# Kernel optimization log

Measured on AMD Instinct MI355X. Metric: run time of the kernel, lower is better.

Reference implementation:

```python
import jax, jax.numpy as jnp
import numpy as np

EPS = 1e-7
LN_EPS = 1e-5

# Lorentz model, points represented by spatial coords x in R^dim; time coord t = sqrt(K + ||x||^2), K = 1/c.

def log_map_zero(x, c):
    K = 1.0 / c
    sqrtK = jnp.sqrt(K)
    xnorm = jnp.linalg.norm(x, axis=-1, keepdims=True)
    t = jnp.sqrt(K + xnorm * xnorm)
    theta = jnp.arccosh(jnp.maximum(t / sqrtK, 1.0 + EPS))
    return sqrtK * theta * x / jnp.maximum(xnorm, EPS)


def exp_map_zero(v, c):
    K = 1.0 / c
    sqrtK = jnp.sqrt(K)
    vnorm = jnp.linalg.norm(v, axis=-1, keepdims=True)
    return sqrtK * jnp.sinh(vnorm / sqrtK) * v / jnp.maximum(vnorm, EPS)


def layer_norm(x, gamma, beta):
    mu = jnp.mean(x, axis=-1, keepdims=True)
    var = jnp.mean((x - mu) ** 2, axis=-1, keepdims=True)
    return (x - mu) * jax.lax.rsqrt(var + LN_EPS) * gamma + beta


def setup_inputs() -> dict:
    key = jax.random.key(0)
    N, D, E, L = 50000, 128, 800000, 2
    ks = jax.random.split(key, 8)
    x_hyp = jax.random.normal(ks[0], (N, D), dtype=jnp.float32)
    edge_index = jax.random.randint(ks[1], (2, E), 0, N, dtype=jnp.int64)
    W = jax.random.normal(ks[2], (L, D, D), dtype=jnp.float32) / np.sqrt(D)
    b = jnp.zeros((L, D), dtype=jnp.float32)
    gamma = jnp.ones((L, D), dtype=jnp.float32)
    beta = jnp.zeros((L, D), dtype=jnp.float32)
    curv = jnp.ones((L,), dtype=jnp.float32)
    return {"x_hyp": x_hyp, "edge_index": edge_index, "W": W, "b": b,
            "gamma": gamma, "beta": beta, "curv": curv}


def reference(x_hyp, edge_index, W, b, gamma, beta, curv):
    N = x_hyp.shape[0]
    L = W.shape[0]
    src, dst = edge_index[0], edge_index[1]
    # in-degree counts for mean aggregation (clamped to avoid div by 0)
    counts = jax.ops.segment_sum(jnp.ones_like(dst, dtype=x_hyp.dtype), dst, num_segments=N)
    counts = jnp.maximum(counts, 1.0)[:, None]
    x = x_hyp
    for l in range(L):
        # curvature treated as constant (torch uses .item())
        c = jax.lax.stop_gradient(jnp.clip(curv[l], 0.1, 10.0))
        x_tan = log_map_zero(x, c)                      # [N, D]
        x_lin = x_tan @ W[l].T + b[l]                   # [N, D]
        msgs = x_lin[src]                               # [E, D] gather
        agg = jax.ops.segment_sum(msgs, dst, num_segments=N) / counts  # scatter-mean
        x_tan_out = layer_norm(x_tan + agg, gamma[l], beta[l])  # dropout in eval mode
        x = exp_map_zero(x_tan_out, c)
    return x
```

## Files before the change

### kernel.cpp

```cpp
#include <hip/hip_runtime.h>
#include <hip/hip_bf16.h>

typedef __attribute__((ext_vector_type(4))) float f32x4;
typedef __attribute__((ext_vector_type(2))) float f32x2;
typedef __attribute__((ext_vector_type(8))) short bf16x8;

constexpr int D = 128;
constexpr int SB = 256;
constexpr int K4CAP = 8192;
#define FEPS 1e-7f
#define FLN_EPS 1e-5f

__device__ __forceinline__ float groupReduceSum16(float x) {
#pragma unroll
  for (int off = 1; off < 16; off <<= 1) x += __shfl_xor(x, off, 64);
  return x;
}

__device__ __forceinline__ unsigned short f2bf(float x) {
  unsigned int u = __float_as_uint(x);
  u += 0x7fffu + ((u >> 16) & 1u);
  return (unsigned short)(u >> 16);
}

__device__ __forceinline__ unsigned int pack2(float a, float b) {
  return (unsigned int)f2bf(a) | ((unsigned int)f2bf(b) << 16);
}

__device__ __forceinline__ f32x2 unp(unsigned int x) {
  f32x2 r;
  r.x = __uint_as_float(x << 16);
  r.y = __uint_as_float(x & 0xffff0000u);
  return r;
}

__device__ __forceinline__ void accp(f32x2* A, uint4 u) {
  A[0] += unp(u.x);
  A[1] += unp(u.y);
  A[2] += unp(u.z);
  A[3] += unp(u.w);
}


__global__ __launch_bounds__(1024) void k2_scan(int* __restrict__ bh,
                                                int* __restrict__ bucket_base, int NB, int E) {
  __shared__ int bsum[256];
  int tid = threadIdx.x, lane = tid & 63, wv = tid >> 6;
  for (int bin = wv; bin < NB; bin += 16) {
    int carry = 0;
    int* row = bh + bin * SB;
#pragma unroll
    for (int sgm = 0; sgm < 4; ++sgm) {
      int v = row[sgm * 64 + lane];
      int x = v;
#pragma unroll
      for (int off = 1; off < 64; off <<= 1) {
        int t = __shfl_up(x, off, 64);
        if (lane >= off) x += t;
      }
      row[sgm * 64 + lane] = carry + x - v;
      carry += __shfl(x, 63, 64);
    }
    if (lane == 0) bsum[bin] = carry;
  }
  __syncthreads();
  if (wv == 0) {
    int carry = 0;
    for (int base = 0; base < NB; base += 64) {
      int v = (base + lane < NB) ? bsum[base + lane] : 0;
      int x = v;
#pragma unroll
      for (int off = 1; off < 64; off <<= 1) {
        int t = __shfl_up(x, off, 64);
        if (lane >= off) x += t;
      }
      if (base + lane < NB) {
        int excl = carry + x - v;
        bsum[base + lane] = excl;
        bucket_base[base + lane] = excl;
      }
      carry += __shfl(x, 63, 64);
    }
    if (lane == 0) bucket_base[NB] = E;
  }
  __syncthreads();
  for (int bin = wv; bin < NB; bin += 16) {
    int bb = bsum[bin];
    int* row = bh + bin * SB;
    for (int s = lane; s < SB; s += 64) row[s] += bb;
  }
}

__global__ __launch_bounds__(1024) void k3_scatter(const int* __restrict__ src,
                                                   const int* __restrict__ dst,
                                                   const int* __restrict__ bh,
                                                   unsigned int* __restrict__ ebuf, int E,
                                                   int NB, int chunk) {
  __shared__ int base[256];
  __shared__ int cur[256];
  int tid = threadIdx.x;
  if (tid < 256) {
    base[tid] = (tid < NB) ? bh[tid * SB + blockIdx.x] : 0;
    cur[tid] = 0;
  }
  __syncthreads();
  int e0 = blockIdx.x * chunk;
  int e1 = min(e0 + chunk, E);
  for (int e = e0 + tid; e < e1; e += 1024) {
    int d = dst[e];
    int s = src[e];
    int bin = d >> 8;
    int r = atomicAdd(&cur[bin], 1);
    ebuf[base[bin] + r] = (unsigned int)(s & 0xffff) | ((unsigned int)(d & 255) << 16);
  }
}

__global__ __launch_bounds__(1024) void k4_csr(const unsigned int* __restrict__ ebuf,
                                               const int* __restrict__ bucket_base,
                                               int* __restrict__ rowptr,
                                               unsigned short* __restrict__ col, int N, int NB,
                                               int E) {
  __shared__ unsigned int stash[K4CAP];
  __shared__ int hist[256];
  __shared__ int cur[256];
  int b = blockIdx.x, tid = threadIdx.x;
  int e0 = bucket_base[b], e1 = bucket_base[b + 1];
  int cnt = e1 - e0;
  if (tid < 256) {
    hist[tid] = 0;
    cur[tid] = 0;
  }
  __syncthreads();
  for (int i = tid; i < cnt; i += 1024) {
    unsigned int u = ebuf[e0 + i];
    if (i < K4CAP) stash[i] = u;
    atomicAdd(&hist[u >> 16], 1);
  }
  __syncthreads();
  int lane = tid & 63;
  if (tid < 64) {
    int carry = 0;
#pragma unroll
    for (int sgm = 0; sgm < 4; ++sgm) {
      int v = hist[sgm * 64 + lane];
      int x = v;
#pragma unroll
      for (int off = 1; off < 64; off <<= 1) {
        int t = __shfl_up(x, off, 64);
        if (lane >= off) x += t;
      }
      hist[sgm * 64 + lane] = carry + x - v;
      carry += __shfl(x, 63, 64);
    }
  }
  __syncthreads();
  int node0 = b << 8;
  if (tid < 256 && node0 + tid < N) rowptr[node0 + tid] = e0 + hist[tid];
  if (b == 0 && tid == 0) rowptr[N] = E;
  for (int i = tid; i < cnt; i += 1024) {
    unsigned int u = (i < K4CAP) ? stash[i] : ebuf[e0 + i];
    int slot = u >> 16;
    int r = atomicAdd(&cur[slot], 1);
    col[e0 + hist[slot] + r] = (unsigned short)(u & 0xffff);
  }
}


template <int FIRST>
__device__ __forceinline__ void gemm_body1024(int gbid, unsigned short* Wlds,
                                              const float* __restrict__ xf,
                                              const unsigned short* __restrict__ A,
                                              const float* __restrict__ Wf,
                                              const float* __restrict__ bias,
                                              const float* __restrict__ curv, int l,
                                              unsigned short* __restrict__ xt,
                                              unsigned short* __restrict__ xl, int N) {
  const float* Wp = Wf + (size_t)l * D * D;
  for (int idx = threadIdx.x; idx < 2048; idx += 1024) {
    int lanei = idx & 63, kbt = idx >> 6;
    int kb = kbt & 3, tcol = kbt >> 2;
    int g = lanei >> 4, r = lanei & 15;
    const float* s = Wp + (size_t)(tcol * 16 + r) * D + kb * 32 + g * 8;
    float4 f0 = *reinterpret_cast<const float4*>(s);
    float4 f1 = *reinterpret_cast<const float4*>(s + 4);
    uint4 u;
    u.x = pack2(f0.x, f0.y);
    u.y = pack2(f0.z, f0.w);
    u.z = pack2(f1.x, f1.y);
    u.w = pack2(f1.z, f1.w);
    *reinterpret_cast<uint4*>(&Wlds[idx * 8]) = u;
  }
  __syncthreads();
  int lane = threadIdx.x & 63;
  int trow = gbid * 16 + (threadIdx.x >> 6);
  int n0 = trow * 16;
  if (n0 >= N) return;
  int g = lane >> 4, r = lane & 15;
  int ar = n0 + r;
  if (ar > N - 1) ar = N - 1;

  bf16x8 af[4];
  if (FIRST) {
    float c = fminf(fmaxf(curv[l], 0.1f), 10.0f);
    float K = 1.0f / c, sqrtK = sqrtf(K);
    float4 fa[4][2];
    float ss = 0.f;
#pragma unroll
    for (int kb = 0; kb < 4; ++kb) {
      const float4* xr = reinterpret_cast<const float4*>(xf + (size_t)ar * D + kb * 32 + g * 8);
      fa[kb][0] = xr[0];
      fa[kb][1] = xr[1];
      ss += fa[kb][0].x * fa[kb][0].x + fa[kb][0].y * fa[kb][0].y +
            fa[kb][0].z * fa[kb][0].z + fa[kb][0].w * fa[kb][0].w;
      ss += fa[kb][1].x * fa[kb][1].x + fa[kb][1].y * fa[kb][1].y +
            fa[kb][1].z * fa[kb][1].z + fa[kb][1].w * fa[kb][1].w;
    }
    ss += __shfl_xor(ss, 16, 64);
    ss += __shfl_xor(ss, 32, 64);
    float xnorm = sqrtf(ss);
    float t = sqrtf(K + ss);
    float theta = acoshf(fmaxf(t / sqrtK, 1.0f + FEPS));
    float scale = sqrtK * theta / fmaxf(xnorm, FEPS);
#pragma unroll
    for (int kb = 0; kb < 4; ++kb) {
      union { bf16x8 v; uint4 u; } cv;
      cv.u.x = pack2(fa[kb][0].x * scale, fa[kb][0].y * scale);
      cv.u.y = pack2(fa[kb][0].z * scale, fa[kb][0].w * scale);
      cv.u.z = pack2(fa[kb][1].x * scale, fa[kb][1].y * scale);
      cv.u.w = pack2(fa[kb][1].z * scale, fa[kb][1].w * scale);
      af[kb] = cv.v;
      *reinterpret_cast<uint4*>(xt + (size_t)ar * D + kb * 32 + g * 8) = cv.u;
    }
  } else {
#pragma unroll
    for (int kb = 0; kb < 4; ++kb)
      af[kb] = *reinterpret_cast<const bf16x8*>(A + (size_t)ar * D + kb * 32 + g * 8);
  }

  int colj = lane & 15, rb = (lane >> 4) * 4;
#pragma unroll
  for (int tcol = 0; tcol < 8; ++tcol) {
    f32x4 acc = {0.f, 0.f, 0.f, 0.f};
#pragma unroll
    for (int kb = 0; kb < 4; ++kb) {
      bf16x8 bfm = *reinterpret_cast<const bf16x8*>(&Wlds[((tcol * 4 + kb) * 64 + lane) * 8]);
      acc = __builtin_amdgcn_mfma_f32_16x16x32_bf16(af[kb], bfm, acc, 0, 0, 0);
    }
    float bv = bias[l * D + tcol * 16 + colj];
#pragma unroll
    for (int i = 0; i < 4; ++i) {
      int row = n0 + rb + i;
      if (row < N) xl[(size_t)row * D + tcol * 16 + colj] = f2bf(acc[i] + bv);
    }
  }
}

__global__ __launch_bounds__(1024) void fusedA_kernel(const int* __restrict__ dst,
                                                      int* __restrict__ bh, int E, int NB,
                                                      int chunk, const float* __restrict__ xf,
                                                      const float* __restrict__ Wf,
                                                      const float* __restrict__ bias,
                                                      const float* __restrict__ curv,
                                                      unsigned short* __restrict__ xt,
                                                      unsigned short* __restrict__ xl, int N) {
  __shared__ unsigned short Wlds[128 * 128];
  int bid = blockIdx.x;
  if (bid < SB) {
    int* h = (int*)Wlds;
    int tid = threadIdx.x;
    if (tid < 256) h[tid] = 0;
    __syncthreads();
    int e0 = bid * chunk;
    int e1 = min(e0 + chunk, E);
    for (int e = e0 + tid; e < e1; e += 1024) atomicAdd(&h[dst[e] >> 8], 1);
    __syncthreads();
    if (tid < NB) bh[tid * SB + bid] = h[tid];
  } else {
    gemm_body1024<1>(bid - SB, Wlds, xf, nullptr, Wf, bias, curv, 0, xt, xl, N);
  }
}

__global__ __launch_bounds__(1024) void gemm_kernel(const unsigned short* __restrict__ A,
                                                    const float* __restrict__ Wf,
                                                    const float* __restrict__ bias,
                                                    const float* __restrict__ curv, int l,
                                                    unsigned short* __restrict__ xl, int N) {
  __shared__ unsigned short Wlds[128 * 128];
  gemm_body1024<0>(blockIdx.x, Wlds, nullptr, A, Wf, bias, curv, l, nullptr, xl, N);
}


template <int MODE>
__global__ __launch_bounds__(256) void agg_kernel(const unsigned short* __restrict__ xl,
                                                  unsigned short* __restrict__ xt,
                                                  const int* __restrict__ rowptr,
                                                  const unsigned short* __restrict__ col,
                                                  const float* __restrict__ gamma,
                                                  const float* __restrict__ beta,
                                                  const float* __restrict__ curv, int l,
                                                  float* __restrict__ out, int N) {
  int tid = threadIdx.x;
  int lane = tid & 63;
  int gl = lane & 15, g = lane >> 4;
  int wid = tid >> 6;
  int node = blockIdx.x * 16 + wid * 4 + g;
  bool active = node < N;
  int nd = active ? node : N - 1;

  float c = fminf(fmaxf(curv[l], 0.1f), 10.0f);
  float K = 1.0f / c, sqrtK = sqrtf(K);

  int e0 = rowptr[nd], e1 = rowptr[nd + 1];
  int deg = e1 - e0;
  const unsigned short* cb = col + e0;

  f32x2 A0[4], A1[4], A2[4], A3[4];
#pragma unroll
  for (int j = 0; j < 4; ++j) {
    A0[j] = 0.f;
    A1[j] = 0.f;
    A2[j] = 0.f;
    A3[j] = 0.f;
  }

  const uint4* xlp = reinterpret_cast<const uint4*>(xl);
  for (int base = 0; base < deg; base += 16) {
    int cidx = (base + gl < deg) ? (int)cb[base + gl] : 0;
    int m = deg - base;
    if (m > 16) m = 16;
    int k = 0;
    for (; k + 8 <= m; k += 8) {
      uint4 u[8];
#pragma unroll
      for (int t = 0; t < 8; ++t) {
        int s = __shfl(cidx, g * 16 + k + t, 64);
        u[t] = xlp[(size_t)s * 16 + gl];
      }
      accp(A0, u[0]);
      accp(A1, u[1]);
      accp(A2, u[2]);
      accp(A3, u[3]);
      accp(A0, u[4]);
      accp(A1, u[5]);
      accp(A2, u[6]);
      accp(A3, u[7]);
    }
    for (; k + 2 <= m; k += 2) {
      int s0 = __shfl(cidx, g * 16 + k, 64);
      int s1 = __shfl(cidx, g * 16 + k + 1, 64);
      uint4 u0 = xlp[(size_t)s0 * 16 + gl];
      uint4 u1 = xlp[(size_t)s1 * 16 + gl];
      accp(A0, u0);
      accp(A1, u1);
    }
    if (k < m) {
      int s0 = __shfl(cidx, g * 16 + k, 64);
      uint4 u0 = xlp[(size_t)s0 * 16 + gl];
      accp(A0, u0);
    }
  }
  f32x2 AV[4];
#pragma unroll
  for (int j = 0; j < 4; ++j) AV[j] = (A0[j] + A1[j]) + (A2[j] + A3[j]);

  float inv = 1.f / fmaxf((float)deg, 1.f);
  uint4 ut = reinterpret_cast<const uint4*>(xt)[(size_t)nd * 16 + gl];
  f32x2 utv[4];
  utv[0] = unp(ut.x);
  utv[1] = unp(ut.y);
  utv[2] = unp(ut.z);
  utv[3] = unp(ut.w);
  float v[8];
#pragma unroll
  for (int j = 0; j < 4; ++j) {
    v[2 * j] = utv[j].x + AV[j].x * inv;
    v[2 * j + 1] = utv[j].y + AV[j].y * inv;
  }

  float s1 = 0.f, s2 = 0.f;
#pragma unroll
  for (int j = 0; j < 8; ++j) { s1 += v[j]; s2 += v[j] * v[j]; }
  s1 = groupReduceSum16(s1);
  s2 = groupReduceSum16(s2);
  float mu = s1 * (1.f / 128.f);
  float var = fmaxf(s2 * (1.f / 128.f) - mu * mu, 0.f);
  float rstd = rsqrtf(var + FLN_EPS);

  float4 gm0 = *reinterpret_cast<const float4*>(gamma + l * D + gl * 8);
  float4 gm1 = *reinterpret_cast<const float4*>(gamma + l * D + gl * 8 + 4);
  float4 bt0 = *reinterpret_cast<const float4*>(beta + l * D + gl * 8);
  float4 bt1 = *reinterpret_cast<const float4*>(beta + l * D + gl * 8 + 4);
  float y[8];
  y[0] = (v[0] - mu) * rstd * gm0.x + bt0.x;
  y[1] = (v[1] - mu) * rstd * gm0.y + bt0.y;
  y[2] = (v[2] - mu) * rstd * gm0.z + bt0.z;
  y[3] = (v[3] - mu) * rstd * gm0.w + bt0.w;
  y[4] = (v[4] - mu) * rstd * gm1.x + bt1.x;
  y[5] = (v[5] - mu) * rstd * gm1.y + bt1.y;
  y[6] = (v[6] - mu) * rstd * gm1.z + bt1.z;
  y[7] = (v[7] - mu) * rstd * gm1.w + bt1.w;

  float ss = 0.f;
#pragma unroll
  for (int j = 0; j < 8; ++j) ss += y[j] * y[j];
  ss = groupReduceSum16(ss);
  float vn = sqrtf(ss);
  float sc = sqrtK * sinhf(vn / sqrtK) / fmaxf(vn, FEPS);

  if (MODE == 0) {
    if (active) {
      float4 o0, o1;
      o0.x = y[0] * sc; o0.y = y[1] * sc; o0.z = y[2] * sc; o0.w = y[3] * sc;
      o1.x = y[4] * sc; o1.y = y[5] * sc; o1.z = y[6] * sc; o1.w = y[7] * sc;
      float4* op = reinterpret_cast<float4*>(out + (size_t)node * D + gl * 8);
      op[0] = o0;
      op[1] = o1;
    }
  } else {
    float xn = sqrtK * sinhf(vn / sqrtK);
    float c2 = fminf(fmaxf(curv[l + 1], 0.1f), 10.0f);
    float K2 = 1.0f / c2, sqrtK2 = sqrtf(K2);
    float t2 = sqrtf(K2 + xn * xn);
    float theta = acoshf(fmaxf(t2 / sqrtK2, 1.0f + FEPS));
    float sc2 = sqrtK2 * theta / fmaxf(xn, FEPS);
    float st = sc * sc2;
    if (active) {
      uint4 w;
      w.x = pack2(y[0] * st, y[1] * st);
      w.y = pack2(y[2] * st, y[3] * st);
      w.z = pack2(y[4] * st, y[5] * st);
      w.w = pack2(y[6] * st, y[7] * st);
      reinterpret_cast<uint4*>(xt)[(size_t)node * 16 + gl] = w;
    }
  }
}


extern "C" void kernel_launch(void* const* d_in, const int* in_sizes, int n_in,
                              void* d_out, int out_size, void* d_ws, size_t ws_size,
                              hipStream_t stream) {
  const float* x_hyp = (const float*)d_in[0];
  const int* edge = (const int*)d_in[1];
  const float* W = (const float*)d_in[2];
  const float* b = (const float*)d_in[3];
  const float* gamma = (const float*)d_in[4];
  const float* beta = (const float*)d_in[5];
  const float* curv = (const float*)d_in[6];
  float* out = (float*)d_out;
  int N = in_sizes[0] / D;
  int E = in_sizes[1] / 2;
  int L = in_sizes[6];
  const int* src = edge;
  const int* dst = edge + E;

  char* p = (char*)d_ws;
  auto alloc = [&](size_t bytes) {
    char* r = p;
    p += (bytes + 255) & ~(size_t)255;
    return r;
  };
  int NB = (N + 255) >> 8;
  int chunk = (E + SB - 1) / SB;

  int* bh = (int*)alloc((size_t)256 * SB * 4);
  int* bucket_base = (int*)alloc((size_t)(NB + 1) * 4);
  unsigned int* ebuf = (unsigned int*)alloc((size_t)E * 4);
  int* rowptr = (int*)alloc((size_t)(N + 1) * 4);
  unsigned short* colp = (unsigned short*)alloc((size_t)E * 2);
  unsigned short* xt16 = (unsigned short*)alloc((size_t)N * D * 2);
  unsigned short* xl16 = (unsigned short*)alloc((size_t)N * D * 2);

  int g1024 = ((N + 15) / 16 + 15) / 16;

  fusedA_kernel<<<SB + g1024, 1024, 0, stream>>>(dst, bh, E, NB, chunk, x_hyp, W, b, curv,
                                                 xt16, xl16, N);
  k2_scan<<<1, 1024, 0, stream>>>(bh, bucket_base, NB, E);
  k3_scatter<<<SB, 1024, 0, stream>>>(src, dst, bh, ebuf, E, NB, chunk);
  k4_csr<<<NB, 1024, 0, stream>>>(ebuf, bucket_base, rowptr, colp, N, NB, E);

  for (int l = 0; l < L; ++l) {
    if (l > 0) {
      gemm_kernel<<<g1024, 1024, 0, stream>>>(xt16, W, b, curv, l, xl16, N);
    }
    if (l < L - 1) {
      agg_kernel<1><<<(N + 15) / 16, 256, 0, stream>>>(xl16, xt16, rowptr, colp, gamma, beta,
                                                       curv, l, out, N);
    } else {
      agg_kernel<0><<<(N + 15) / 16, 256, 0, stream>>>(xl16, xt16, rowptr, colp, gamma, beta,
                                                       curv, l, out, N);
    }
  }
}
```

Measured before the change: 151.4 us.

## Fuse next-layer GEMM into aggregation epilogue with ping-pong buffers

Removes the separate layer-1 GEMM kernel. The aggregation kernel now stages its 16-node bf16 tangent tile in LDS and runs the MFMA projection for the next layer in its epilogue. Next-layer weights are pre-converted to bf16 by an extra block in the first fused kernel, and ping-pong buffers keep the read and write xl arrays separate. The accumulator layout is also changed to split even and odd lanes, avoiding per-element unpacking shuffles. The cost is a block barrier, LDS use and weight reads from global/L2 in every aggregation block.

```diff
diff --git a/kernel.cpp b/kernel.cpp
--- a/kernel.cpp
+++ b/kernel.cpp
@@ -34,11 +34,24 @@
   return r;
 }
 
-__device__ __forceinline__ void accp(f32x2* A, uint4 u) {
-  A[0] += unp(u.x);
-  A[1] += unp(u.y);
-  A[2] += unp(u.z);
-  A[3] += unp(u.w);
+struct AccSet {
+  f32x2 e0, o0, e1, o1;
+};
+
+__device__ __forceinline__ void accu(AccSet& s, uint4 u) {
+  f32x2 t;
+  t.x = __uint_as_float(u.x << 16);
+  t.y = __uint_as_float(u.y << 16);
+  s.e0 += t;
+  t.x = __uint_as_float(u.x);
+  t.y = __uint_as_float(u.y);
+  s.o0 += t;
+  t.x = __uint_as_float(u.z << 16);
+  t.y = __uint_as_float(u.w << 16);
+  s.e1 += t;
+  t.x = __uint_as_float(u.z);
+  t.y = __uint_as_float(u.w);
+  s.o1 += t;
 }
 
 
@@ -166,16 +179,14 @@
 }
 
 
-template <int FIRST>
-__device__ __forceinline__ void gemm_body1024(int gbid, unsigned short* Wlds,
-                                              const float* __restrict__ xf,
-                                              const unsigned short* __restrict__ A,
-                                              const float* __restrict__ Wf,
-                                              const float* __restrict__ bias,
-                                              const float* __restrict__ curv, int l,
-                                              unsigned short* __restrict__ xt,
-                                              unsigned short* __restrict__ xl, int N) {
-  const float* Wp = Wf + (size_t)l * D * D;
+__device__ __forceinline__ void gemm0_body(int gbid, unsigned short* Wlds,
+                                           const float* __restrict__ xf,
+                                           const float* __restrict__ Wf,
+                                           const float* __restrict__ bias,
+                                           const float* __restrict__ curv,
+                                           unsigned short* __restrict__ xt,
+                                           unsigned short* __restrict__ xl, int N) {
+  const float* Wp = Wf;
   for (int idx = threadIdx.x; idx < 2048; idx += 1024) {
     int lanei = idx & 63, kbt = idx >> 6;
     int kb = kbt & 3, tcol = kbt >> 2;
@@ -200,41 +211,35 @@
   if (ar > N - 1) ar = N - 1;
 
   bf16x8 af[4];
-  if (FIRST) {
-    float c = fminf(fmaxf(curv[l], 0.1f), 10.0f);
-    float K = 1.0f / c, sqrtK = sqrtf(K);
-    float4 fa[4][2];
-    float ss = 0.f;
-#pragma unroll
-    for (int kb = 0; kb < 4; ++kb) {
-      const float4* xr = reinterpret_cast<const float4*>(xf + (size_t)ar * D + kb * 32 + g * 8);
-      fa[kb][0] = xr[0];
-      fa[kb][1] = xr[1];
-      ss += fa[kb][0].x * fa[kb][0].x + fa[kb][0].y * fa[kb][0].y +
-            fa[kb][0].z * fa[kb][0].z + fa[kb][0].w * fa[kb][0].w;
-      ss += fa[kb][1].x * fa[kb][1].x + fa[kb][1].y * fa[kb][1].y +
-            fa[kb][1].z * fa[kb][1].z + fa[kb][1].w * fa[kb][1].w;
-    }
-    ss += __shfl_xor(ss, 16, 64);
-    ss += __shfl_xor(ss, 32, 64);
-    float xnorm = sqrtf(ss);
-    float t = sqrtf(K + ss);
-    float theta = acoshf(fmaxf(t / sqrtK, 1.0f + FEPS));
-    float scale = sqrtK * theta / fmaxf(xnorm, FEPS);
-#pragma unroll
-    for (int kb = 0; kb < 4; ++kb) {
-      union { bf16x8 v; uint4 u; } cv;
-      cv.u.x = pack2(fa[kb][0].x * scale, fa[kb][0].y * scale);
-      cv.u.y = pack2(fa[kb][0].z * scale, fa[kb][0].w * scale);
-      cv.u.z = pack2(fa[kb][1].x * scale, fa[kb][1].y * scale);
-      cv.u.w = pack2(fa[kb][1].z * scale, fa[kb][1].w * scale);
-      af[kb] = cv.v;
-      *reinterpret_cast<uint4*>(xt + (size_t)ar * D + kb * 32 + g * 8) = cv.u;
-    }
-  } else {
-#pragma unroll
-    for (int kb = 0; kb < 4; ++kb)
-      af[kb] = *reinterpret_cast<const bf16x8*>(A + (size_t)ar * D + kb * 32 + g * 8);
+  float c = fminf(fmaxf(curv[0], 0.1f), 10.0f);
+  float K = 1.0f / c, sqrtK = sqrtf(K);
+  float4 fa[4][2];
+  float ss = 0.f;
+#pragma unroll
+  for (int kb = 0; kb < 4; ++kb) {
+    const float4* xr = reinterpret_cast<const float4*>(xf + (size_t)ar * D + kb * 32 + g * 8);
+    fa[kb][0] = xr[0];
+    fa[kb][1] = xr[1];
+    ss += fa[kb][0].x * fa[kb][0].x + fa[kb][0].y * fa[kb][0].y + fa[kb][0].z * fa[kb][0].z +
+          fa[kb][0].w * fa[kb][0].w;
+    ss += fa[kb][1].x * fa[kb][1].x + fa[kb][1].y * fa[kb][1].y + fa[kb][1].z * fa[kb][1].z +
+          fa[kb][1].w * fa[kb][1].w;
+  }
+  ss += __shfl_xor(ss, 16, 64);
+  ss += __shfl_xor(ss, 32, 64);
+  float xnorm = sqrtf(ss);
+  float t = sqrtf(K + ss);
+  float theta = acoshf(fmaxf(t / sqrtK, 1.0f + FEPS));
+  float scale = sqrtK * theta / fmaxf(xnorm, FEPS);
+#pragma unroll
+  for (int kb = 0; kb < 4; ++kb) {
+    union { bf16x8 v; uint4 u; } cv;
+    cv.u.x = pack2(fa[kb][0].x * scale, fa[kb][0].y * scale);
+    cv.u.y = pack2(fa[kb][0].z * scale, fa[kb][0].w * scale);
+    cv.u.z = pack2(fa[kb][1].x * scale, fa[kb][1].y * scale);
+    cv.u.w = pack2(fa[kb][1].z * scale, fa[kb][1].w * scale);
+    af[kb] = cv.v;
+    *reinterpret_cast<uint4*>(xt + (size_t)ar * D + kb * 32 + g * 8) = cv.u;
   }
 
   int colj = lane & 15, rb = (lane >> 4) * 4;
@@ -246,7 +251,7 @@
       bf16x8 bfm = *reinterpret_cast<const bf16x8*>(&Wlds[((tcol * 4 + kb) * 64 + lane) * 8]);
       acc = __builtin_amdgcn_mfma_f32_16x16x32_bf16(af[kb], bfm, acc, 0, 0, 0);
     }
-    float bv = bias[l * D + tcol * 16 + colj];
+    float bv = bias[tcol * 16 + colj];
 #pragma unroll
     for (int i = 0; i < 4; ++i) {
       int row = n0 + rb + i;
@@ -262,7 +267,9 @@
                                                       const float* __restrict__ bias,
                                                       const float* __restrict__ curv,
                                                       unsigned short* __restrict__ xt,
-                                                      unsigned short* __restrict__ xl, int N) {
+                                                      unsigned short* __restrict__ xl, int N,
+                                                      unsigned short* __restrict__ W16,
+                                                      int nconv, int gblocks) {
   __shared__ unsigned short Wlds[128 * 128];
   int bid = blockIdx.x;
   if (bid < SB) {
@@ -275,30 +282,33 @@
     for (int e = e0 + tid; e < e1; e += 1024) atomicAdd(&h[dst[e] >> 8], 1);
     __syncthreads();
     if (tid < NB) bh[tid * SB + bid] = h[tid];
+  } else if (bid < SB + gblocks) {
+    gemm0_body(bid - SB, Wlds, xf, Wf, bias, curv, xt, xl, N);
   } else {
-    gemm_body1024<1>(bid - SB, Wlds, xf, nullptr, Wf, bias, curv, 0, xt, xl, N);
-  }
-}
-
-__global__ __launch_bounds__(1024) void gemm_kernel(const unsigned short* __restrict__ A,
-                                                    const float* __restrict__ Wf,
-                                                    const float* __restrict__ bias,
-                                                    const float* __restrict__ curv, int l,
-                                                    unsigned short* __restrict__ xl, int N) {
-  __shared__ unsigned short Wlds[128 * 128];
-  gemm_body1024<0>(blockIdx.x, Wlds, nullptr, A, Wf, bias, curv, l, nullptr, xl, N);
+    for (int i = threadIdx.x * 4; i < nconv; i += 4096) {
+      float4 f = *reinterpret_cast<const float4*>(Wf + D * D + i);
+      uint2 o;
+      o.x = pack2(f.x, f.y);
+      o.y = pack2(f.z, f.w);
+      *reinterpret_cast<uint2*>(W16 + i) = o;
+    }
+  }
 }
 
 
 template <int MODE>
-__global__ __launch_bounds__(256) void agg_kernel(const unsigned short* __restrict__ xl,
+__global__ __launch_bounds__(256) void agg_kernel(const unsigned short* __restrict__ xl_in,
                                                   unsigned short* __restrict__ xt,
                                                   const int* __restrict__ rowptr,
                                                   const unsigned short* __restrict__ col,
                                                   const float* __restrict__ gamma,
                                                   const float* __restrict__ beta,
                                                   const float* __restrict__ curv, int l,
+                                                  const unsigned short* __restrict__ W16n,
+                                                  const float* __restrict__ bias,
+                                                  unsigned short* __restrict__ xl_out,
                                                   float* __restrict__ out, int N) {
+  __shared__ unsigned short xtile[16 * 136];
   int tid = threadIdx.x;
   int lane = tid & 63;
   int gl = lane & 15, g = lane >> 4;
@@ -314,16 +324,16 @@
   int deg = e1 - e0;
   const unsigned short* cb = col + e0;
 
-  f32x2 A0[4], A1[4], A2[4], A3[4];
+  AccSet S[4];
 #pragma unroll
   for (int j = 0; j < 4; ++j) {
-    A0[j] = 0.f;
-    A1[j] = 0.f;
-    A2[j] = 0.f;
-    A3[j] = 0.f;
-  }
-
-  const uint4* xlp = reinterpret_cast<const uint4*>(xl);
+    S[j].e0 = 0.f;
+    S[j].o0 = 0.f;
+    S[j].e1 = 0.f;
+    S[j].o1 = 0.f;
+  }
+
+  const uint4* xlp = reinterpret_cast<const uint4*>(xl_in);
   for (int base = 0; base < deg; base += 16) {
     int cidx = (base + gl < deg) ? (int)cb[base + gl] : 0;
     int m = deg - base;
@@ -336,32 +346,28 @@
         int s = __shfl(cidx, g * 16 + k + t, 64);
         u[t] = xlp[(size_t)s * 16 + gl];
       }
-      accp(A0, u[0]);
-      accp(A1, u[1]);
-      accp(A2, u[2]);
-      accp(A3, u[3]);
-      accp(A0, u[4]);
-      accp(A1, u[5]);
-      accp(A2, u[6]);
-      accp(A3, u[7]);
+#pragma unroll
+      for (int t = 0; t < 8; ++t) accu(S[t & 3], u[t]);
     }
     for (; k + 2 <= m; k += 2) {
       int s0 = __shfl(cidx, g * 16 + k, 64);
       int s1 = __shfl(cidx, g * 16 + k + 1, 64);
       uint4 u0 = xlp[(size_t)s0 * 16 + gl];
       uint4 u1 = xlp[(size_t)s1 * 16 + gl];
-      accp(A0, u0);
-      accp(A1, u1);
+      accu(S[0], u0);
+      accu(S[1], u1);
     }
     if (k < m) {
       int s0 = __shfl(cidx, g * 16 + k, 64);
       uint4 u0 = xlp[(size_t)s0 * 16 + gl];
-      accp(A0, u0);
-    }
-  }
-  f32x2 AV[4];
-#pragma unroll
-  for (int j = 0; j < 4; ++j) AV[j] = (A0[j] + A1[j]) + (A2[j] + A3[j]);
+      accu(S[0], u0);
+    }
+  }
+  f32x2 E0 = (S[0].e0 + S[1].e0) + (S[2].e0 + S[3].e0);
+  f32x2 O0 = (S[0].o0 + S[1].o0) + (S[2].o0 + S[3].o0);
+  f32x2 E1 = (S[0].e1 + S[1].e1) + (S[2].e1 + S[3].e1);
+  f32x2 O1 = (S[0].o1 + S[1].o1) + (S[2].o1 + S[3].o1);
+  float a[8] = {E0.x, O0.x, E0.y, O0.y, E1.x, O1.x, E1.y, O1.y};
 
   float inv = 1.f / fmaxf((float)deg, 1.f);
   uint4 ut = reinterpret_cast<const uint4*>(xt)[(size_t)nd * 16 + gl];
@@ -373,13 +379,16 @@
   float v[8];
 #pragma unroll
   for (int j = 0; j < 4; ++j) {
-    v[2 * j] = utv[j].x + AV[j].x * inv;
-    v[2 * j + 1] = utv[j].y + AV[j].y * inv;
+    v[2 * j] = utv[j].x + a[2 * j] * inv;
+    v[2 * j + 1] = utv[j].y + a[2 * j + 1] * inv;
   }
 
   float s1 = 0.f, s2 = 0.f;
 #pragma unroll
-  for (int j = 0; j < 8; ++j) { s1 += v[j]; s2 += v[j] * v[j]; }
+  for (int j = 0; j < 8; ++j) {
+    s1 += v[j];
+    s2 += v[j] * v[j];
+  }
   s1 = groupReduceSum16(s1);
   s2 = groupReduceSum16(s2);
   float mu = s1 * (1.f / 128.f);
@@ -410,8 +419,14 @@
   if (MODE == 0) {
     if (active) {
       float4 o0, o1;
-      o0.x = y[0] * sc; o0.y = y[1] * sc; o0.z = y[2] * sc; o0.w = y[3] * sc;
-      o1.x = y[4] * sc; o1.y = y[5] * sc; o1.z = y[6] * sc; o1.w = y[7] * sc;
+      o0.x = y[0] * sc;
+      o0.y = y[1] * sc;
+      o0.z = y[2] * sc;
+      o0.w = y[3] * sc;
+      o1.x = y[4] * sc;
+      o1.y = y[5] * sc;
+      o1.z = y[6] * sc;
+      o1.w = y[7] * sc;
       float4* op = reinterpret_cast<float4*>(out + (size_t)node * D + gl * 8);
       op[0] = o0;
       op[1] = o1;
@@ -424,13 +439,39 @@
     float theta = acoshf(fmaxf(t2 / sqrtK2, 1.0f + FEPS));
     float sc2 = sqrtK2 * theta / fmaxf(xn, FEPS);
     float st = sc * sc2;
-    if (active) {
-      uint4 w;
-      w.x = pack2(y[0] * st, y[1] * st);
-      w.y = pack2(y[2] * st, y[3] * st);
-      w.z = pack2(y[4] * st, y[5] * st);
-      w.w = pack2(y[6] * st, y[7] * st);
-      reinterpret_cast<uint4*>(xt)[(size_t)node * 16 + gl] = w;
+    uint4 w;
+    w.x = pack2(y[0] * st, y[1] * st);
+    w.y = pack2(y[2] * st, y[3] * st);
+    w.z = pack2(y[4] * st, y[5] * st);
+    w.w = pack2(y[6] * st, y[7] * st);
+    int noderow = wid * 4 + g;
+    *reinterpret_cast<uint4*>(&xtile[noderow * 136 + gl * 8]) = w;
+    if (active) reinterpret_cast<uint4*>(xt)[(size_t)node * 16 + gl] = w;
+    __syncthreads();
+
+    int rr = lane & 15, kg = lane >> 4;
+    bf16x8 af[4];
+#pragma unroll
+    for (int kb = 0; kb < 4; ++kb)
+      af[kb] = *reinterpret_cast<const bf16x8*>(&xtile[rr * 136 + kb * 32 + kg * 8]);
+    int n0 = blockIdx.x * 16;
+    int rb = kg * 4;
+#pragma unroll
+    for (int t = 0; t < 2; ++t) {
+      int tcol = wid * 2 + t;
+      f32x4 acc = {0.f, 0.f, 0.f, 0.f};
+#pragma unroll
+      for (int kb = 0; kb < 4; ++kb) {
+        bf16x8 bfm = *reinterpret_cast<const bf16x8*>(W16n + (size_t)(tcol * 16 + rr) * D +
+                                                      kb * 32 + kg * 8);
+        acc = __builtin_amdgcn_mfma_f32_16x16x32_bf16(af[kb], bfm, acc, 0, 0, 0);
+      }
+      float bv = bias[(l + 1) * D + tcol * 16 + rr];
+#pragma unroll
+      for (int i = 0; i < 4; ++i) {
+        int row = n0 + rb + i;
+        if (row < N) xl_out[(size_t)row * D + tcol * 16 + rr] = f2bf(acc[i] + bv);
+      }
     }
   }
 }
@@ -468,26 +509,32 @@
   int* rowptr = (int*)alloc((size_t)(N + 1) * 4);
   unsigned short* colp = (unsigned short*)alloc((size_t)E * 2);
   unsigned short* xt16 = (unsigned short*)alloc((size_t)N * D * 2);
-  unsigned short* xl16 = (unsigned short*)alloc((size_t)N * D * 2);
+  unsigned short* xlA = (unsigned short*)alloc((size_t)N * D * 2);
+  unsigned short* xlB = (unsigned short*)alloc((size_t)N * D * 2);
+  unsigned short* W16 = (unsigned short*)alloc((size_t)(L > 1 ? (L - 1) : 1) * D * D * 2);
 
   int g1024 = ((N + 15) / 16 + 15) / 16;
-
-  fusedA_kernel<<<SB + g1024, 1024, 0, stream>>>(dst, bh, E, NB, chunk, x_hyp, W, b, curv,
-                                                 xt16, xl16, N);
+  int nconv = (L - 1) * D * D;
+
+  fusedA_kernel<<<SB + g1024 + 1, 1024, 0, stream>>>(dst, bh, E, NB, chunk, x_hyp, W, b, curv,
+                                                     xt16, xlA, N, W16, nconv, g1024);
   k2_scan<<<1, 1024, 0, stream>>>(bh, bucket_base, NB, E);
   k3_scatter<<<SB, 1024, 0, stream>>>(src, dst, bh, ebuf, E, NB, chunk);
   k4_csr<<<NB, 1024, 0, stream>>>(ebuf, bucket_base, rowptr, colp, N, NB, E);
 
+  unsigned short* xl_cur = xlA;
+  unsigned short* xl_nxt = xlB;
   for (int l = 0; l < L; ++l) {
-    if (l > 0) {
-      gemm_kernel<<<g1024, 1024, 0, stream>>>(xt16, W, b, curv, l, xl16, N);
-    }
     if (l < L - 1) {
-      agg_kernel<1><<<(N + 15) / 16, 256, 0, stream>>>(xl16, xt16, rowptr, colp, gamma, beta,
-                                                       curv, l, out, N);
+      agg_kernel<1><<<(N + 15) / 16, 256, 0, stream>>>(
+          xl_cur, xt16, rowptr, colp, gamma, beta, curv, l, W16 + (size_t)l * D * D, b, xl_nxt,
+          out, N);
+      unsigned short* tmp = xl_cur;
+      xl_cur = xl_nxt;
+      xl_nxt = tmp;
     } else {
-      agg_kernel<0><<<(N + 15) / 16, 256, 0, stream>>>(xl16, xt16, rowptr, colp, gamma, beta,
-                                                       curv, l, out, N);
-    }
-  }
-}
+      agg_kernel<0><<<(N + 15) / 16, 256, 0, stream>>>(xl_cur, xt16, rowptr, colp, gamma, beta,
+                                                       curv, l, nullptr, b, nullptr, out, N);
+    }
+  }
+}
```

New measurement: 149.6 us. No clear change (-1.2%).

## Aggregate before linear transform and fuse GEMM into aggregation kernel

Applied to the files above, without the earlier changes.

Applies the linear layer after the mean aggregation rather than before, using mean(xW+b) = mean(x)W + b·[deg>0]. Each agg block first gathers neighbour x_tan rows, splits the mean into bf16 hi and lo parts, and runs MFMA against a bf16 copy of W inside the block before LayerNorm. This drops the separate GEMM kernels and the xl intermediate buffer and its write/read traffic. It adds LDS use and W loads per block, and the histogram and scatter launches are reorganised, with the log-map and W conversion moved into the scatter launch.

```diff
diff --git a/kernel.cpp b/kernel.cpp
--- a/kernel.cpp
+++ b/kernel.cpp
@@ -41,6 +41,19 @@
   A[3] += unp(u.w);
 }
 
+
+__global__ __launch_bounds__(1024) void k1_hist(const int* __restrict__ dst,
+                                                int* __restrict__ bh, int E, int NB, int chunk) {
+  __shared__ int h[256];
+  int tid = threadIdx.x;
+  if (tid < 256) h[tid] = 0;
+  __syncthreads();
+  int e0 = blockIdx.x * chunk;
+  int e1 = min(e0 + chunk, E);
+  for (int e = e0 + tid; e < e1; e += 1024) atomicAdd(&h[dst[e] >> 8], 1);
+  __syncthreads();
+  if (tid < NB) bh[tid * SB + blockIdx.x] = h[tid];
+}
 
 __global__ __launch_bounds__(1024) void k2_scan(int* __restrict__ bh,
                                                 int* __restrict__ bucket_base, int NB, int E) {
@@ -88,30 +101,6 @@
     int bb = bsum[bin];
     int* row = bh + bin * SB;
     for (int s = lane; s < SB; s += 64) row[s] += bb;
-  }
-}
-
-__global__ __launch_bounds__(1024) void k3_scatter(const int* __restrict__ src,
-                                                   const int* __restrict__ dst,
-                                                   const int* __restrict__ bh,
-                                                   unsigned int* __restrict__ ebuf, int E,
-                                                   int NB, int chunk) {
-  __shared__ int base[256];
-  __shared__ int cur[256];
-  int tid = threadIdx.x;
-  if (tid < 256) {
-    base[tid] = (tid < NB) ? bh[tid * SB + blockIdx.x] : 0;
-    cur[tid] = 0;
-  }
-  __syncthreads();
-  int e0 = blockIdx.x * chunk;
-  int e1 = min(e0 + chunk, E);
-  for (int e = e0 + tid; e < e1; e += 1024) {
-    int d = dst[e];
-    int s = src[e];
-    int bin = d >> 8;
-    int r = atomicAdd(&cur[bin], 1);
-    ebuf[base[bin] + r] = (unsigned int)(s & 0xffff) | ((unsigned int)(d & 255) << 16);
   }
 }
 
@@ -166,139 +155,84 @@
 }
 
 
-template <int FIRST>
-__device__ __forceinline__ void gemm_body1024(int gbid, unsigned short* Wlds,
-                                              const float* __restrict__ xf,
-                                              const unsigned short* __restrict__ A,
-                                              const float* __restrict__ Wf,
-                                              const float* __restrict__ bias,
-                                              const float* __restrict__ curv, int l,
-                                              unsigned short* __restrict__ xt,
-                                              unsigned short* __restrict__ xl, int N) {
-  const float* Wp = Wf + (size_t)l * D * D;
-  for (int idx = threadIdx.x; idx < 2048; idx += 1024) {
-    int lanei = idx & 63, kbt = idx >> 6;
-    int kb = kbt & 3, tcol = kbt >> 2;
-    int g = lanei >> 4, r = lanei & 15;
-    const float* s = Wp + (size_t)(tcol * 16 + r) * D + kb * 32 + g * 8;
-    float4 f0 = *reinterpret_cast<const float4*>(s);
-    float4 f1 = *reinterpret_cast<const float4*>(s + 4);
-    uint4 u;
-    u.x = pack2(f0.x, f0.y);
-    u.y = pack2(f0.z, f0.w);
-    u.z = pack2(f1.x, f1.y);
-    u.w = pack2(f1.z, f1.w);
-    *reinterpret_cast<uint4*>(&Wlds[idx * 8]) = u;
-  }
-  __syncthreads();
-  int lane = threadIdx.x & 63;
-  int trow = gbid * 16 + (threadIdx.x >> 6);
-  int n0 = trow * 16;
-  if (n0 >= N) return;
-  int g = lane >> 4, r = lane & 15;
-  int ar = n0 + r;
-  if (ar > N - 1) ar = N - 1;
-
-  bf16x8 af[4];
-  if (FIRST) {
-    float c = fminf(fmaxf(curv[l], 0.1f), 10.0f);
+__global__ __launch_bounds__(1024) void bundle_kernel(
+    const int* __restrict__ src, const int* __restrict__ dst, const int* __restrict__ bh,
+    unsigned int* __restrict__ ebuf, int E, int NB, int chunk, const float* __restrict__ xf,
+    const float* __restrict__ Wf, const float* __restrict__ curv,
+    unsigned short* __restrict__ xt, int N, unsigned short* __restrict__ W16, int nconv,
+    int lmblocks) {
+  __shared__ int scratch[512];
+  int bid = blockIdx.x;
+  int tid = threadIdx.x;
+  if (bid < SB) {
+    int* base = scratch;
+    int* cur = scratch + 256;
+    if (tid < 256) {
+      base[tid] = (tid < NB) ? bh[tid * SB + bid] : 0;
+      cur[tid] = 0;
+    }
+    __syncthreads();
+    int e0 = bid * chunk;
+    int e1 = min(e0 + chunk, E);
+    for (int e = e0 + tid; e < e1; e += 1024) {
+      int d = dst[e];
+      int s = src[e];
+      int bin = d >> 8;
+      int r = atomicAdd(&cur[bin], 1);
+      ebuf[base[bin] + r] = (unsigned int)(s & 0xffff) | ((unsigned int)(d & 255) << 16);
+    }
+  } else if (bid < SB + lmblocks) {
+    int lane = tid & 63, wv = tid >> 6;
+    int gl = lane & 15, g = lane >> 4;
+    int row = (bid - SB) * 64 + wv * 4 + g;
+    bool active = row < N;
+    int rd = active ? row : N - 1;
+    float c = fminf(fmaxf(curv[0], 0.1f), 10.0f);
     float K = 1.0f / c, sqrtK = sqrtf(K);
-    float4 fa[4][2];
-    float ss = 0.f;
-#pragma unroll
-    for (int kb = 0; kb < 4; ++kb) {
-      const float4* xr = reinterpret_cast<const float4*>(xf + (size_t)ar * D + kb * 32 + g * 8);
-      fa[kb][0] = xr[0];
-      fa[kb][1] = xr[1];
-      ss += fa[kb][0].x * fa[kb][0].x + fa[kb][0].y * fa[kb][0].y +
-            fa[kb][0].z * fa[kb][0].z + fa[kb][0].w * fa[kb][0].w;
-      ss += fa[kb][1].x * fa[kb][1].x + fa[kb][1].y * fa[kb][1].y +
-            fa[kb][1].z * fa[kb][1].z + fa[kb][1].w * fa[kb][1].w;
-    }
-    ss += __shfl_xor(ss, 16, 64);
-    ss += __shfl_xor(ss, 32, 64);
+    const float4* xr = reinterpret_cast<const float4*>(xf + (size_t)rd * D + gl * 8);
+    float4 f0 = xr[0];
+    float4 f1 = xr[1];
+    float ss = f0.x * f0.x + f0.y * f0.y + f0.z * f0.z + f0.w * f0.w + f1.x * f1.x +
+               f1.y * f1.y + f1.z * f1.z + f1.w * f1.w;
+    ss = groupReduceSum16(ss);
     float xnorm = sqrtf(ss);
     float t = sqrtf(K + ss);
     float theta = acoshf(fmaxf(t / sqrtK, 1.0f + FEPS));
     float scale = sqrtK * theta / fmaxf(xnorm, FEPS);
-#pragma unroll
-    for (int kb = 0; kb < 4; ++kb) {
-      union { bf16x8 v; uint4 u; } cv;
-      cv.u.x = pack2(fa[kb][0].x * scale, fa[kb][0].y * scale);
-      cv.u.y = pack2(fa[kb][0].z * scale, fa[kb][0].w * scale);
-      cv.u.z = pack2(fa[kb][1].x * scale, fa[kb][1].y * scale);
-      cv.u.w = pack2(fa[kb][1].z * scale, fa[kb][1].w * scale);
-      af[kb] = cv.v;
-      *reinterpret_cast<uint4*>(xt + (size_t)ar * D + kb * 32 + g * 8) = cv.u;
+    if (active) {
+      uint4 w;
+      w.x = pack2(f0.x * scale, f0.y * scale);
+      w.y = pack2(f0.z * scale, f0.w * scale);
+      w.z = pack2(f1.x * scale, f1.y * scale);
+      w.w = pack2(f1.z * scale, f1.w * scale);
+      reinterpret_cast<uint4*>(xt)[(size_t)row * 16 + gl] = w;
     }
   } else {
-#pragma unroll
-    for (int kb = 0; kb < 4; ++kb)
-      af[kb] = *reinterpret_cast<const bf16x8*>(A + (size_t)ar * D + kb * 32 + g * 8);
-  }
-
-  int colj = lane & 15, rb = (lane >> 4) * 4;
-#pragma unroll
-  for (int tcol = 0; tcol < 8; ++tcol) {
-    f32x4 acc = {0.f, 0.f, 0.f, 0.f};
-#pragma unroll
-    for (int kb = 0; kb < 4; ++kb) {
-      bf16x8 bfm = *reinterpret_cast<const bf16x8*>(&Wlds[((tcol * 4 + kb) * 64 + lane) * 8]);
-      acc = __builtin_amdgcn_mfma_f32_16x16x32_bf16(af[kb], bfm, acc, 0, 0, 0);
-    }
-    float bv = bias[l * D + tcol * 16 + colj];
-#pragma unroll
-    for (int i = 0; i < 4; ++i) {
-      int row = n0 + rb + i;
-      if (row < N) xl[(size_t)row * D + tcol * 16 + colj] = f2bf(acc[i] + bv);
-    }
-  }
-}
-
-__global__ __launch_bounds__(1024) void fusedA_kernel(const int* __restrict__ dst,
-                                                      int* __restrict__ bh, int E, int NB,
-                                                      int chunk, const float* __restrict__ xf,
-                                                      const float* __restrict__ Wf,
-                                                      const float* __restrict__ bias,
-                                                      const float* __restrict__ curv,
-                                                      unsigned short* __restrict__ xt,
-                                                      unsigned short* __restrict__ xl, int N) {
-  __shared__ unsigned short Wlds[128 * 128];
-  int bid = blockIdx.x;
-  if (bid < SB) {
-    int* h = (int*)Wlds;
-    int tid = threadIdx.x;
-    if (tid < 256) h[tid] = 0;
-    __syncthreads();
-    int e0 = bid * chunk;
-    int e1 = min(e0 + chunk, E);
-    for (int e = e0 + tid; e < e1; e += 1024) atomicAdd(&h[dst[e] >> 8], 1);
-    __syncthreads();
-    if (tid < NB) bh[tid * SB + bid] = h[tid];
-  } else {
-    gemm_body1024<1>(bid - SB, Wlds, xf, nullptr, Wf, bias, curv, 0, xt, xl, N);
-  }
-}
-
-__global__ __launch_bounds__(1024) void gemm_kernel(const unsigned short* __restrict__ A,
-                                                    const float* __restrict__ Wf,
-                                                    const float* __restrict__ bias,
-                                                    const float* __restrict__ curv, int l,
-                                                    unsigned short* __restrict__ xl, int N) {
-  __shared__ unsigned short Wlds[128 * 128];
-  gemm_body1024<0>(blockIdx.x, Wlds, nullptr, A, Wf, bias, curv, l, nullptr, xl, N);
+    for (int i = tid * 4; i < nconv; i += 4096) {
+      float4 f = *reinterpret_cast<const float4*>(Wf + i);
+      uint2 o;
+      o.x = pack2(f.x, f.y);
+      o.y = pack2(f.z, f.w);
+      *reinterpret_cast<uint2*>(W16 + i) = o;
+    }
+  }
 }
 
 
 template <int MODE>
-__global__ __launch_bounds__(256) void agg_kernel(const unsigned short* __restrict__ xl,
-                                                  unsigned short* __restrict__ xt,
+__global__ __launch_bounds__(256) void agg_kernel(const unsigned short* __restrict__ xt_in,
+                                                  unsigned short* __restrict__ xt_out,
                                                   const int* __restrict__ rowptr,
                                                   const unsigned short* __restrict__ col,
                                                   const float* __restrict__ gamma,
                                                   const float* __restrict__ beta,
                                                   const float* __restrict__ curv, int l,
+                                                  const unsigned short* __restrict__ Wl,
+                                                  const float* __restrict__ bias,
                                                   float* __restrict__ out, int N) {
+  __shared__ unsigned short xhi[16 * 136];
+  __shared__ unsigned short xlo[16 * 136];
+  __shared__ float ztile[16 * 132];
   int tid = threadIdx.x;
   int lane = tid & 63;
   int gl = lane & 15, g = lane >> 4;
@@ -314,72 +248,130 @@
   int deg = e1 - e0;
   const unsigned short* cb = col + e0;
 
-  f32x2 A0[4], A1[4], A2[4], A3[4];
+  f32x2 A0[4], A1[4];
 #pragma unroll
   for (int j = 0; j < 4; ++j) {
     A0[j] = 0.f;
     A1[j] = 0.f;
-    A2[j] = 0.f;
-    A3[j] = 0.f;
-  }
-
-  const uint4* xlp = reinterpret_cast<const uint4*>(xl);
+  }
+
+  const uint4* xtp = reinterpret_cast<const uint4*>(xt_in);
+  int cidx = (gl < deg) ? (int)cb[gl] : 0;
   for (int base = 0; base < deg; base += 16) {
-    int cidx = (base + gl < deg) ? (int)cb[base + gl] : 0;
+    int nb = base + 16;
+    int cnext = (nb + gl < deg) ? (int)cb[nb + gl] : 0;
     int m = deg - base;
     if (m > 16) m = 16;
     int k = 0;
-    for (; k + 8 <= m; k += 8) {
-      uint4 u[8];
-#pragma unroll
-      for (int t = 0; t < 8; ++t) {
-        int s = __shfl(cidx, g * 16 + k + t, 64);
-        u[t] = xlp[(size_t)s * 16 + gl];
-      }
-      accp(A0, u[0]);
-      accp(A1, u[1]);
-      accp(A2, u[2]);
-      accp(A3, u[3]);
-      accp(A0, u[4]);
-      accp(A1, u[5]);
-      accp(A2, u[6]);
-      accp(A3, u[7]);
-    }
-    for (; k + 2 <= m; k += 2) {
+    for (; k + 4 <= m; k += 4) {
       int s0 = __shfl(cidx, g * 16 + k, 64);
       int s1 = __shfl(cidx, g * 16 + k + 1, 64);
-      uint4 u0 = xlp[(size_t)s0 * 16 + gl];
-      uint4 u1 = xlp[(size_t)s1 * 16 + gl];
+      int s2 = __shfl(cidx, g * 16 + k + 2, 64);
+      int s3 = __shfl(cidx, g * 16 + k + 3, 64);
+      uint4 u0 = xtp[(size_t)s0 * 16 + gl];
+      uint4 u1 = xtp[(size_t)s1 * 16 + gl];
+      uint4 u2 = xtp[(size_t)s2 * 16 + gl];
+      uint4 u3 = xtp[(size_t)s3 * 16 + gl];
       accp(A0, u0);
       accp(A1, u1);
-    }
-    if (k < m) {
+      accp(A0, u2);
+      accp(A1, u3);
+    }
+    for (; k < m; ++k) {
       int s0 = __shfl(cidx, g * 16 + k, 64);
-      uint4 u0 = xlp[(size_t)s0 * 16 + gl];
+      uint4 u0 = xtp[(size_t)s0 * 16 + gl];
       accp(A0, u0);
     }
-  }
-  f32x2 AV[4];
-#pragma unroll
-  for (int j = 0; j < 4; ++j) AV[j] = (A0[j] + A1[j]) + (A2[j] + A3[j]);
+    cidx = cnext;
+  }
+  float a[8];
+#pragma unroll
+  for (int j = 0; j < 4; ++j) {
+    f32x2 t = A0[j] + A1[j];
+    a[2 * j] = t.x;
+    a[2 * j + 1] = t.y;
+  }
 
   float inv = 1.f / fmaxf((float)deg, 1.f);
-  uint4 ut = reinterpret_cast<const uint4*>(xt)[(size_t)nd * 16 + gl];
+  float flag = (deg > 0) ? 1.f : 0.f;
+
+  int noderow = wid * 4 + g;
+  {
+    uint4 whi, wlo;
+    unsigned int hb[8];
+    float lo[8];
+#pragma unroll
+    for (int j = 0; j < 8; ++j) {
+      float mj = a[j] * inv;
+      unsigned short h = f2bf(mj);
+      hb[j] = h;
+      lo[j] = mj - __uint_as_float(((unsigned int)h) << 16);
+    }
+    whi.x = hb[0] | (hb[1] << 16);
+    whi.y = hb[2] | (hb[3] << 16);
+    whi.z = hb[4] | (hb[5] << 16);
+    whi.w = hb[6] | (hb[7] << 16);
+    wlo.x = pack2(lo[0], lo[1]);
+    wlo.y = pack2(lo[2], lo[3]);
+    wlo.z = pack2(lo[4], lo[5]);
+    wlo.w = pack2(lo[6], lo[7]);
+    *reinterpret_cast<uint4*>(&xhi[noderow * 136 + gl * 8]) = whi;
+    *reinterpret_cast<uint4*>(&xlo[noderow * 136 + gl * 8]) = wlo;
+  }
+  __syncthreads();
+
+  {
+    int rr = lane & 15, kg = lane >> 4;
+    bf16x8 ah[4], al[4];
+#pragma unroll
+    for (int kb = 0; kb < 4; ++kb) {
+      ah[kb] = *reinterpret_cast<const bf16x8*>(&xhi[rr * 136 + kb * 32 + kg * 8]);
+      al[kb] = *reinterpret_cast<const bf16x8*>(&xlo[rr * 136 + kb * 32 + kg * 8]);
+    }
+#pragma unroll
+    for (int t = 0; t < 2; ++t) {
+      int tcol = wid * 2 + t;
+      f32x4 acc = {0.f, 0.f, 0.f, 0.f};
+#pragma unroll
+      for (int kb = 0; kb < 4; ++kb) {
+        bf16x8 bfm = *reinterpret_cast<const bf16x8*>(Wl + (size_t)(tcol * 16 + rr) * D +
+                                                      kb * 32 + kg * 8);
+        acc = __builtin_amdgcn_mfma_f32_16x16x32_bf16(ah[kb], bfm, acc, 0, 0, 0);
+        acc = __builtin_amdgcn_mfma_f32_16x16x32_bf16(al[kb], bfm, acc, 0, 0, 0);
+      }
+#pragma unroll
+      for (int i = 0; i < 4; ++i) ztile[(kg * 4 + i) * 132 + tcol * 16 + rr] = acc[i];
+    }
+  }
+  __syncthreads();
+
+  float4 wm0 = *reinterpret_cast<const float4*>(&ztile[noderow * 132 + gl * 8]);
+  float4 wm1 = *reinterpret_cast<const float4*>(&ztile[noderow * 132 + gl * 8 + 4]);
+  float4 bi0 = *reinterpret_cast<const float4*>(bias + l * D + gl * 8);
+  float4 bi1 = *reinterpret_cast<const float4*>(bias + l * D + gl * 8 + 4);
+
+  uint4 ut = xtp[(size_t)nd * 16 + gl];
   f32x2 utv[4];
   utv[0] = unp(ut.x);
   utv[1] = unp(ut.y);
   utv[2] = unp(ut.z);
   utv[3] = unp(ut.w);
   float v[8];
-#pragma unroll
-  for (int j = 0; j < 4; ++j) {
-    v[2 * j] = utv[j].x + AV[j].x * inv;
-    v[2 * j + 1] = utv[j].y + AV[j].y * inv;
-  }
+  v[0] = utv[0].x + wm0.x + bi0.x * flag;
+  v[1] = utv[0].y + wm0.y + bi0.y * flag;
+  v[2] = utv[1].x + wm0.z + bi0.z * flag;
+  v[3] = utv[1].y + wm0.w + bi0.w * flag;
+  v[4] = utv[2].x + wm1.x + bi1.x * flag;
+  v[5] = utv[2].y + wm1.y + bi1.y * flag;
+  v[6] = utv[3].x + wm1.z + bi1.z * flag;
+  v[7] = utv[3].y + wm1.w + bi1.w * flag;
 
   float s1 = 0.f, s2 = 0.f;
 #pragma unroll
-  for (int j = 0; j < 8; ++j) { s1 += v[j]; s2 += v[j] * v[j]; }
+  for (int j = 0; j < 8; ++j) {
+    s1 += v[j];
+    s2 += v[j] * v[j];
+  }
   s1 = groupReduceSum16(s1);
   s2 = groupReduceSum16(s2);
   float mu = s1 * (1.f / 128.f);
@@ -410,8 +402,14 @@
   if (MODE == 0) {
     if (active) {
       float4 o0, o1;
-      o0.x = y[0] * sc; o0.y = y[1] * sc; o0.z = y[2] * sc; o0.w = y[3] * sc;
-      o1.x = y[4] * sc; o1.y = y[5] * sc; o1.z = y[6] * sc; o1.w = y[7] * sc;
+      o0.x = y[0] * sc;
+      o0.y = y[1] * sc;
+      o0.z = y[2] * sc;
+      o0.w = y[3] * sc;
+      o1.x = y[4] * sc;
+      o1.y = y[5] * sc;
+      o1.z = y[6] * sc;
+      o1.w = y[7] * sc;
       float4* op = reinterpret_cast<float4*>(out + (size_t)node * D + gl * 8);
       op[0] = o0;
       op[1] = o1;
@@ -430,7 +428,7 @@
       w.y = pack2(y[2] * st, y[3] * st);
       w.z = pack2(y[4] * st, y[5] * st);
       w.w = pack2(y[6] * st, y[7] * st);
-      reinterpret_cast<uint4*>(xt)[(size_t)node * 16 + gl] = w;
+      reinterpret_cast<uint4*>(xt_out)[(size_t)node * 16 + gl] = w;
     }
   }
 }
@@ -467,27 +465,34 @@
   unsigned int* ebuf = (unsigned int*)alloc((size_t)E * 4);
   int* rowptr = (int*)alloc((size_t)(N + 1) * 4);
   unsigned short* colp = (unsigned short*)alloc((size_t)E * 2);
-  unsigned short* xt16 = (unsigned short*)alloc((size_t)N * D * 2);
-  unsigned short* xl16 = (unsigned short*)alloc((size_t)N * D * 2);
-
-  int g1024 = ((N + 15) / 16 + 15) / 16;
-
-  fusedA_kernel<<<SB + g1024, 1024, 0, stream>>>(dst, bh, E, NB, chunk, x_hyp, W, b, curv,
-                                                 xt16, xl16, N);
+  unsigned short* xtA = (unsigned short*)alloc((size_t)N * D * 2);
+  unsigned short* xtB = (unsigned short*)alloc((size_t)N * D * 2);
+  unsigned short* W16 = (unsigned short*)alloc((size_t)L * D * D * 2);
+
+  int lmblocks = (N + 63) / 64;
+  int nconv = L * D * D;
+
+  k1_hist<<<SB, 1024, 0, stream>>>(dst, bh, E, NB, chunk);
   k2_scan<<<1, 1024, 0, stream>>>(bh, bucket_base, NB, E);
-  k3_scatter<<<SB, 1024, 0, stream>>>(src, dst, bh, ebuf, E, NB, chunk);
+  bundle_kernel<<<SB + lmblocks + 1, 1024, 0, stream>>>(src, dst, bh, ebuf, E, NB, chunk,
+                                                        x_hyp, W, curv, xtA, N, W16, nconv,
+                                                        lmblocks);
   k4_csr<<<NB, 1024, 0, stream>>>(ebuf, bucket_base, rowptr, colp, N, NB, E);
 
+  unsigned short* cur = xtA;
+  unsigned short* nxt = xtB;
   for (int l = 0; l < L; ++l) {
-    if (l > 0) {
-      gemm_kernel<<<g1024, 1024, 0, stream>>>(xt16, W, b, curv, l, xl16, N);
-    }
     if (l < L - 1) {
-      agg_kernel<1><<<(N + 15) / 16, 256, 0, stream>>>(xl16, xt16, rowptr, colp, gamma, beta,
-                                                       curv, l, out, N);
+      agg_kernel<1><<<(N + 15) / 16, 256, 0, stream>>>(cur, nxt, rowptr, colp, gamma, beta,
+                                                       curv, l, W16 + (size_t)l * D * D, b,
+                                                       out, N);
+      unsigned short* tmp = cur;
+      cur = nxt;
+      nxt = tmp;
     } else {
-      agg_kernel<0><<<(N + 15) / 16, 256, 0, stream>>>(xl16, xt16, rowptr, colp, gamma, beta,
-                                                       curv, l, out, N);
-    }
-  }
-}
+      agg_kernel<0><<<(N + 15) / 16, 256, 0, stream>>>(cur, nullptr, rowptr, colp, gamma, beta,
+                                                       curv, l, W16 + (size_t)l * D * D, b,
+                                                       out, N);
+    }
+  }
+}
```

Result: faster. 144.6 us (-4.5%).
